# Kernel optimization log

Hardware: AMD Instinct MI355X
Metric: run time of the kernel (lower is better)

The kernel has to match this reference:

```python
import jax, jax.numpy as jnp
import numpy as np


def setup_inputs() -> dict:
    key = jax.random.key(0)
    k1, k2, k3 = jax.random.split(key, 3)
    B, C, H, W = 8, 256, 64, 64
    K = jax.random.normal(k1, (B, C, H, W), dtype=jnp.float32)
    Q = jax.random.normal(k2, (B, C, H, W), dtype=jnp.float32)
    V = jax.random.normal(k3, (B, C, H, W), dtype=jnp.float32)
    return {"K": K, "Q": Q, "V": V}


def reference(K, Q, V):
    # K, Q: [b, dim, h, w]; V: [b, v_dim, h, w]
    b, dim, h, w = K.shape
    v_dim = V.shape[1]
    hw = h * w
    Qf = jnp.transpose(K.reshape(b, dim, hw), (0, 2, 1)) * 0  # placeholder removed below
    Qf = jnp.transpose(Q.reshape(b, dim, hw), (0, 2, 1))  # [b, hw, dim]
    Kf = K.reshape(b, dim, hw)                              # [b, dim, hw]
    Vf = jnp.transpose(V.reshape(b, v_dim, hw), (0, 2, 1))  # [b, hw, v_dim]
    scores = jnp.einsum('bqd,bdk->bqk', Qf, Kf)             # [b, hw_q, hw_k]
    # NOTE: softmax over the QUERY axis (dim=1), matching the torch code
    att = jax.nn.softmax(scores, axis=1)
    out = jnp.einsum('bqk,bkv->bqv', att, Vf)               # [b, hw, v_dim]
    out = out.reshape(b, h, w, v_dim)
    return jnp.transpose(out, (0, 3, 1, 2))                 # [b, v_dim, h, w]
```

## Files before the change

### kernel.cpp

```cpp
#include <hip/hip_runtime.h>

#define HW   4096
#define DIM  256
#define NB   8

typedef short bf16x8 __attribute__((ext_vector_type(8)));
typedef short s16x4  __attribute__((ext_vector_type(4)));
typedef float f32x4  __attribute__((ext_vector_type(4)));
typedef float f32x16 __attribute__((ext_vector_type(16)));
typedef unsigned int u32_g __attribute__((address_space(1)));
typedef unsigned int u32_l __attribute__((address_space(3)));

__device__ __forceinline__ void split_bf16(float x, short& hi, short& lo) {
    unsigned u  = __builtin_bit_cast(unsigned, x);
    unsigned rh = (u + 0x7FFFu + ((u >> 16) & 1u)) >> 16;
    hi = (short)rh;
    float hf  = __builtin_bit_cast(float, rh << 16);
    float rem = x - hf;
    unsigned u2 = __builtin_bit_cast(unsigned, rem);
    unsigned rl = (u2 + 0x7FFFu + ((u2 >> 16) & 1u)) >> 16;
    lo = (short)rl;
}

__device__ __forceinline__ f32x4 mfma16(bf16x8 a, bf16x8 b, f32x4 c) {
    return __builtin_amdgcn_mfma_f32_16x16x32_bf16(a, b, c, 0, 0, 0);
}
__device__ __forceinline__ f32x16 mfma32(bf16x8 a, bf16x8 b, f32x16 c) {
    return __builtin_amdgcn_mfma_f32_32x32x16_bf16(a, b, c, 0, 0, 0);
}

__device__ __forceinline__ void gload16(const void* g, void* l) {
    __builtin_amdgcn_global_load_lds((const u32_g*)g, (u32_l*)l, 16, 0, 0);
}
__device__ __forceinline__ void gload4(const void* g, void* l) {
    __builtin_amdgcn_global_load_lds((const u32_g*)g, (u32_l*)l, 4, 0, 0);
}

extern "C" __global__ void __launch_bounds__(256)
pass0_T(const float* __restrict__ src, short* __restrict__ dsth,
        short* __restrict__ dstl)
{
    __shared__ __attribute__((aligned(16))) short TH[16][264];
    __shared__ __attribute__((aligned(16))) short TL[16][264];
    const int b   = blockIdx.y;
    const int hw0 = blockIdx.x * 16;
    const int t   = threadIdx.x;
    const float* sb = src + (size_t)b * DIM * HW;

    {
        const int rl = t & 15;
        const int dl = t >> 4;
        #pragma unroll
        for (int dp = 0; dp < 16; ++dp) {
            int d = dl + dp * 16;
            float x = sb[(size_t)d * HW + hw0 + rl];
            short h, l; split_bf16(x, h, l);
            TH[rl][d] = h; TL[rl][d] = l;
        }
    }
    __syncthreads();

    const int r   = t >> 4;
    const int c0  = (t & 15) * 2;
    const int swz = r << 4;
    size_t rowbyte = ((size_t)b * HW + hw0 + r) * (size_t)(DIM * 2);
    char* dh = (char*)dsth + rowbyte;
    char* dl = (char*)dstl + rowbyte;
    #pragma unroll
    for (int j = 0; j < 2; ++j) {
        int cb  = (c0 + j) * 16;
        int cbs = cb ^ swz;
        *(f32x4*)(dh + cbs) = *(const f32x4*)((const char*)&TH[r][0] + cb);
        *(f32x4*)(dl + cbs) = *(const f32x4*)((const char*)&TL[r][0] + cb);
    }
}

extern "C" __global__ void __launch_bounds__(256)
pass0_V(const float* __restrict__ V, short* __restrict__ v2)
{
    const int b = blockIdx.y, v = blockIdx.x, t = threadIdx.x;
    const float* sv = V + ((size_t)b * DIM + v) * HW + t * 16;
    #pragma unroll
    for (int s = 0; s < 2; ++s) {
        f32x4 x0 = *(const f32x4*)(sv + s * 8);
        f32x4 x1 = *(const f32x4*)(sv + s * 8 + 4);
        s16x4 h0, l0, h1, l1;
        #pragma unroll
        for (int j = 0; j < 4; ++j) {
            short h, l;
            split_bf16(x0[j], h, l); h0[j] = h; l0[j] = l;
            split_bf16(x1[j], h, l); h1[j] = h; l1[j] = l;
        }
        short* dp = v2 + (((size_t)b * 512 + (size_t)(t * 2 + s)) * DIM + v) * 16;
        *(s16x4*)(dp + 0)  = h0;
        *(s16x4*)(dp + 4)  = h1;
        *(s16x4*)(dp + 8)  = l0;
        *(s16x4*)(dp + 12) = l1;
    }
}

extern "C" __global__ void __launch_bounds__(512, 2)
k9_stats(const short* __restrict__ KTh, const short* __restrict__ KTl,
         const short* __restrict__ QTh, const short* __restrict__ QTl,
         float* __restrict__ m_out, float* __restrict__ il_out)
{
    __shared__ __attribute__((aligned(16))) short QH[2][64][256];
    __shared__ __attribute__((aligned(16))) short QL[2][64][256];
    __shared__ __attribute__((aligned(16))) float MRG[2][128][2];

    const int id   = blockIdx.x;
    const int b    = id & 7;
    const int k0b  = (id >> 3) * 128;
    const int t    = threadIdx.x;
    const int lane = t & 63;
    const int w    = t >> 6;
    const int l32  = lane & 31;
    const int g2   = lane >> 5;
    const int wk   = w >> 1;
    const int wq   = w & 1;

    bf16x8 kh[16], kl[16];
    {
        const int krow = k0b + wk * 32 + l32;
        const char* rh = (const char*)KTh + ((size_t)b * HW + krow) * 512;
        const char* rl = (const char*)KTl + ((size_t)b * HW + krow) * 512;
        const int swz = (l32 & 15) << 4;
        #pragma unroll
        for (int s = 0; s < 16; ++s) {
            int cb = (s * 32 + g2 * 16) ^ swz;
            kh[s] = *(const bf16x8*)(rh + cb);
            kl[s] = *(const bf16x8*)(rl + cb);
        }
    }

    const char* qhbase = (const char*)QTh + (size_t)b * HW * 512;
    const char* qlbase = (const char*)QTl + (size_t)b * HW * 512;
    auto stage = [&](int bi, int q0s) {
        #pragma unroll
        for (int j = 0; j < 4; ++j) {
            int cc = (j << 3) + w;
            int o  = cc * 1024;
            gload16(qhbase + (size_t)q0s * 512 + o + lane * 16,
                    (char*)&QH[bi][0][0] + o);
            gload16(qlbase + (size_t)q0s * 512 + o + lane * 16,
                    (char*)&QL[bi][0][0] + o);
        }
    };

    const int qrow = wq * 32 + l32;
    const int qswz = (l32 & 15) << 4;

    float mr[16], lr[16];
    #pragma unroll
    for (int r = 0; r < 16; ++r) { mr[r] = -3.0e38f; lr[r] = 0.0f; }

    stage(0, 0);
    __syncthreads();

    for (int it = 0; it < 64; ++it) {
        const int cur = it & 1;
        if (it + 1 < 64) stage(cur ^ 1, (it + 1) * 64);

        const char* bhr = (const char*)&QH[cur][qrow][0];
        const char* blr = (const char*)&QL[cur][qrow][0];
        f32x16 cS;
        #pragma unroll
        for (int e = 0; e < 16; ++e) cS[e] = 0.0f;

        __builtin_amdgcn_s_setprio(1);
        #pragma unroll
        for (int s = 0; s < 16; ++s) {
            int cb = (s * 32 + g2 * 16) ^ qswz;
            bf16x8 bh = *(const bf16x8*)(bhr + cb);
            bf16x8 bl = *(const bf16x8*)(blr + cb);
            cS = mfma32(kh[s], bh, cS);
            cS = mfma32(kh[s], bl, cS);
            cS = mfma32(kl[s], bh, cS);
        }
        __builtin_amdgcn_s_setprio(0);

        #pragma unroll
        for (int r = 0; r < 16; ++r) {
            float sv = cS[r];
            float nm = fmaxf(mr[r], sv);
            lr[r] = lr[r] * __expf(mr[r] - nm) + __expf(sv - nm);
            mr[r] = nm;
        }
        __syncthreads();
    }

    #pragma unroll
    for (int r = 0; r < 16; ++r) {
        float m = mr[r], l = lr[r];
        #pragma unroll
        for (int off = 1; off < 32; off <<= 1) {
            float m2 = __shfl_xor(m, off);
            float l2 = __shfl_xor(l, off);
            float nm = fmaxf(m, m2);
            l = l * __expf(m - nm) + l2 * __expf(m2 - nm);
            m = nm;
        }
        mr[r] = m; lr[r] = l;
    }
    if (l32 == 0) {
        #pragma unroll
        for (int r = 0; r < 16; ++r) {
            int klo = wk * 32 + 4 * g2 + (r & 3) + 8 * (r >> 2);
            MRG[wq][klo][0] = mr[r];
            MRG[wq][klo][1] = lr[r];
        }
    }
    __syncthreads();
    if (t < 128) {
        float m0 = MRG[0][t][0], l0 = MRG[0][t][1];
        float m1 = MRG[1][t][0], l1 = MRG[1][t][1];
        float nm = fmaxf(m0, m1);
        float l  = l0 * __expf(m0 - nm) + l1 * __expf(m1 - nm);
        m_out[b * HW + k0b + t]  = nm;
        il_out[b * HW + k0b + t] = 1.0f / l;
    }
}

extern "C" __global__ void __launch_bounds__(512, 2)
k9_out(const short* __restrict__ KTh, const short* __restrict__ KTl,
       const short* __restrict__ QTh, const short* __restrict__ QTl,
       const short* __restrict__ V2,
       const float* __restrict__ m_in, const float* __restrict__ il_in,
       float* __restrict__ out)
{
    __shared__ __attribute__((aligned(16))) short KH[2][64][256];
    __shared__ __attribute__((aligned(16))) short KL[64][256];
    __shared__ __attribute__((aligned(16))) short PH[128][68];
    __shared__ __attribute__((aligned(16))) short PL[128][68];
    __shared__ __attribute__((aligned(16))) float MI[2][128];

    const int id   = blockIdx.x;
    const int b    = id & 7;
    const int q0   = (id >> 3) * 128;
    const int t    = threadIdx.x;
    const int lane = t & 63;
    const int w    = t >> 6;
    const int l32  = lane & 31;
    const int g2   = lane >> 5;
    const int a    = w & 1;
    const int c    = w >> 1;
    const int wv   = w >> 1;
    const int wq2  = w & 1;

    bf16x8 qh[16], ql[16];
    {
        const int qrow = q0 + c * 32 + l32;
        const char* rh = (const char*)QTh + ((size_t)b * HW + qrow) * 512;
        const char* rl = (const char*)QTl + ((size_t)b * HW + qrow) * 512;
        const int swz = (l32 & 15) << 4;
        #pragma unroll
        for (int s = 0; s < 16; ++s) {
            int cb = (s * 32 + g2 * 16) ^ swz;
            qh[s] = *(const bf16x8*)(rh + cb);
            ql[s] = *(const bf16x8*)(rl + cb);
        }
    }

    const char* khbase = (const char*)KTh + (size_t)b * HW * 512;
    const char* klbase = (const char*)KTl + (size_t)b * HW * 512;
    auto stageKH = [&](int bi, int k0s) {
        #pragma unroll
        for (int j = 0; j < 4; ++j) {
            int cc = (j << 3) + w;
            int o  = cc * 1024;
            gload16(khbase + (size_t)k0s * 512 + o + lane * 16,
                    (char*)&KH[bi][0][0] + o);
        }
    };
    auto stageKL = [&](int k0s) {
        #pragma unroll
        for (int j = 0; j < 4; ++j) {
            int cc = (j << 3) + w;
            int o  = cc * 1024;
            gload16(klbase + (size_t)k0s * 512 + o + lane * 16,
                    (char*)&KL[0][0] + o);
        }
    };
    const float* mB  = m_in  + b * HW;
    const float* ilB = il_in + b * HW;
    auto stageMI = [&](int bi, int k0s) {
        if (w == 0) {
            gload4(mB  + k0s + lane, (char*)&MI[bi][0]);
            gload4(ilB + k0s + lane, (char*)&MI[bi][64]);
        }
    };

    f32x16 acc[2][2];
    #pragma unroll
    for (int i = 0; i < 2; ++i)
        #pragma unroll
        for (int j = 0; j < 2; ++j)
            #pragma unroll
            for (int e = 0; e < 16; ++e) acc[i][j][e] = 0.0f;

    stageKH(0, 0);
    stageKL(0);
    stageMI(0, 0);
    __syncthreads();

    const int arow = a * 32 + l32;
    const int aswz = (l32 & 15) << 4;
    const int prow = c * 32 + l32;

    for (int it = 0; it < 64; ++it) {
        const int cur = it & 1;
        const int k0  = it * 64;

        if (it + 1 < 64) {
            stageKH(cur ^ 1, k0 + 64);
            stageMI(cur ^ 1, k0 + 64);
        }
        bf16x8 v0h[2], v0l[2];
        {
            const int seg = it * 8 + g2;
            #pragma unroll
            for (int mt = 0; mt < 2; ++mt) {
                int v = wv * 64 + mt * 32 + l32;
                const short* vp = V2 + (((size_t)b * 512 + seg) * DIM + v) * 16;
                v0h[mt] = *(const bf16x8*)(vp);
                v0l[mt] = *(const bf16x8*)(vp + 8);
            }
        }

        const char* ahr = (const char*)&KH[cur][arow][0];
        const char* alr = (const char*)&KL[arow][0];
        f32x16 cS;
        #pragma unroll
        for (int e = 0; e < 16; ++e) cS[e] = 0.0f;

        __builtin_amdgcn_s_setprio(1);
        #pragma unroll
        for (int s = 0; s < 16; ++s) {
            int cb = (s * 32 + g2 * 16) ^ aswz;
            bf16x8 ah = *(const bf16x8*)(ahr + cb);
            bf16x8 al = *(const bf16x8*)(alr + cb);
            cS = mfma32(ah, qh[s], cS);
            cS = mfma32(ah, ql[s], cS);
            cS = mfma32(al, qh[s], cS);
        }
        __builtin_amdgcn_s_setprio(0);

        __syncthreads();

        if (it + 1 < 64) stageKL(k0 + 64);

        #pragma unroll
        for (int run = 0; run < 4; ++run) {
            int idx = a * 32 + 4 * g2 + 8 * run;
            f32x4 m4 = *(const f32x4*)&MI[cur][idx];
            f32x4 i4 = *(const f32x4*)&MI[cur][64 + idx];
            s16x4 ph, pl;
            #pragma unroll
            for (int e = 0; e < 4; ++e) {
                int r = run * 4 + e;
                float p = __expf(cS[r] - m4[e]) * i4[e];
                short h, l; split_bf16(p, h, l);
                ph[e] = h; pl[e] = l;
            }
            *(s16x4*)&PH[prow][idx] = ph;
            *(s16x4*)&PL[prow][idx] = pl;
        }

        __syncthreads();

        __builtin_amdgcn_s_setprio(1);
        #pragma unroll
        for (int kc = 0; kc < 4; ++kc) {
            bf16x8 pbh[2], pbl[2];
            #pragma unroll
            for (int qt = 0; qt < 2; ++qt) {
                int pr = wq2 * 64 + qt * 32 + l32;
                const short* p0 = &PH[pr][kc * 16 + g2 * 8];
                const short* p1 = &PL[pr][kc * 16 + g2 * 8];
                s16x4 a0 = *(const s16x4*)(p0);
                s16x4 a1 = *(const s16x4*)(p0 + 4);
                s16x4 b0 = *(const s16x4*)(p1);
                s16x4 b1 = *(const s16x4*)(p1 + 4);
                pbh[qt] = __builtin_shufflevector(a0, a1, 0, 1, 2, 3, 4, 5, 6, 7);
                pbl[qt] = __builtin_shufflevector(b0, b1, 0, 1, 2, 3, 4, 5, 6, 7);
            }
            const int seg = it * 8 + kc * 2 + g2;
            #pragma unroll
            for (int mt = 0; mt < 2; ++mt) {
                bf16x8 vh, vl;
                if (kc == 0) {
                    vh = v0h[mt]; vl = v0l[mt];
                } else {
                    int v = wv * 64 + mt * 32 + l32;
                    const short* vp = V2 + (((size_t)b * 512 + seg) * DIM + v) * 16;
                    vh = *(const bf16x8*)(vp);
                    vl = *(const bf16x8*)(vp + 8);
                }
                #pragma unroll
                for (int qt = 0; qt < 2; ++qt) {
                    acc[mt][qt] = mfma32(vh, pbh[qt], acc[mt][qt]);
                    acc[mt][qt] = mfma32(vh, pbl[qt], acc[mt][qt]);
                    acc[mt][qt] = mfma32(vl, pbh[qt], acc[mt][qt]);
                }
            }
        }
        __builtin_amdgcn_s_setprio(0);
    }

    float* __restrict__ ob = out + (size_t)b * DIM * HW;
    #pragma unroll
    for (int mt = 0; mt < 2; ++mt)
        #pragma unroll
        for (int qt = 0; qt < 2; ++qt)
            #pragma unroll
            for (int r = 0; r < 16; ++r) {
                int v = wv * 64 + mt * 32 + (r & 3) + 8 * (r >> 2) + 4 * g2;
                int q = q0 + wq2 * 64 + qt * 32 + l32;
                ob[(size_t)v * HW + q] = acc[mt][qt][r];
            }
}

extern "C" __global__ void __launch_bounds__(256, 1)
k_stats(const float* __restrict__ K, const float* __restrict__ Q,
        float* __restrict__ m_out, float* __restrict__ il_out)
{
    __shared__ __attribute__((aligned(16))) short KtH[64][264];
    __shared__ __attribute__((aligned(16))) short KtL[64][264];
    __shared__ __attribute__((aligned(16))) short QtH[32][264];
    __shared__ __attribute__((aligned(16))) short QtL[32][264];

    const int b = blockIdx.y, k0 = blockIdx.x * 64, t = threadIdx.x;
    const int lane = t & 63, w = t >> 6, g = lane >> 4, lq = lane & 15;
    const float* Kb = K + (size_t)b * DIM * HW;
    const float* Qb = Q + (size_t)b * DIM * HW;

    {
        const int kk = t & 63, d0 = t >> 6;
        #pragma unroll 4
        for (int pass = 0; pass < 64; ++pass) {
            int d = d0 + pass * 4;
            float x = Kb[(size_t)d * HW + k0 + kk];
            short h, l; split_bf16(x, h, l);
            KtH[kk][d] = h; KtL[kk][d] = l;
        }
    }
    float mr[4], lr[4];
    #pragma unroll
    for (int r = 0; r < 4; ++r) { mr[r] = -3.0e38f; lr[r] = 0.0f; }

    for (int q0 = 0; q0 < HW; q0 += 32) {
        __syncthreads();
        {
            const int qq = t & 31, d0 = t >> 5;
            #pragma unroll 4
            for (int pass = 0; pass < 32; ++pass) {
                int d = d0 + pass * 8;
                float x = Qb[(size_t)d * HW + q0 + qq];
                short h, l; split_bf16(x, h, l);
                QtH[qq][d] = h; QtL[qq][d] = l;
            }
        }
        __syncthreads();
        #pragma unroll
        for (int qt = 0; qt < 2; ++qt) {
            f32x4 acc = {0.f, 0.f, 0.f, 0.f};
            #pragma unroll
            for (int ds = 0; ds < 8; ++ds) {
                const int dof = ds * 32 + g * 8;
                bf16x8 ah = *(const bf16x8*)&KtH[w * 16 + lq][dof];
                bf16x8 al = *(const bf16x8*)&KtL[w * 16 + lq][dof];
                bf16x8 bh = *(const bf16x8*)&QtH[qt * 16 + lq][dof];
                bf16x8 bl = *(const bf16x8*)&QtL[qt * 16 + lq][dof];
                acc = mfma16(ah, bh, acc);
                acc = mfma16(ah, bl, acc);
                acc = mfma16(al, bh, acc);
            }
            #pragma unroll
            for (int r = 0; r < 4; ++r) {
                float s = acc[r];
                if (s > mr[r]) { lr[r] = lr[r] * __expf(mr[r] - s) + 1.0f; mr[r] = s; }
                else lr[r] += __expf(s - mr[r]);
            }
        }
    }
    #pragma unroll
    for (int r = 0; r < 4; ++r) {
        float m = mr[r], l = lr[r];
        #pragma unroll
        for (int off = 1; off < 16; off <<= 1) {
            float m2 = __shfl_xor(m, off), l2 = __shfl_xor(l, off);
            float mn = fmaxf(m, m2);
            l = l * __expf(m - mn) + l2 * __expf(m2 - mn);
            m = mn;
        }
        if (lq == 0) {
            int kg = k0 + w * 16 + g * 4 + r;
            m_out[b * HW + kg] = m;
            il_out[b * HW + kg] = 1.0f / l;
        }
    }
}

extern "C" __global__ void __launch_bounds__(256, 1)
k_attn_out(const float* __restrict__ K, const float* __restrict__ Q,
           const float* __restrict__ V,
           const float* __restrict__ m_in, const float* __restrict__ il_in,
           float* __restrict__ out)
{
    __shared__ __attribute__((aligned(16))) short QtH[64][264];
    __shared__ __attribute__((aligned(16))) short QtL[64][264];
    __shared__ __attribute__((aligned(16))) short KtH[32][264];
    __shared__ __attribute__((aligned(16))) short KtL[32][264];
    __shared__ __attribute__((aligned(16))) short PtH[64][40];
    __shared__ __attribute__((aligned(16))) short PtL[64][40];

    const int b = blockIdx.y, q0 = blockIdx.x * 64, t = threadIdx.x;
    const int lane = t & 63, w = t >> 6, g = lane >> 4, lq = lane & 15;
    const int g2 = lane >> 5, l32 = lane & 31;
    const float* Kb = K + (size_t)b * DIM * HW;
    const float* Qb = Q + (size_t)b * DIM * HW;
    const float* Vb = V + (size_t)b * DIM * HW;
    const float* mB = m_in + b * HW;
    const float* ilB = il_in + b * HW;

    {
        const int qq = t & 63, d0 = t >> 6;
        #pragma unroll 4
        for (int pass = 0; pass < 64; ++pass) {
            int d = d0 + pass * 4;
            float x = Qb[(size_t)d * HW + q0 + qq];
            short h, l; split_bf16(x, h, l);
            QtH[qq][d] = h; QtL[qq][d] = l;
        }
    }
    f32x16 acc[2][2];
    #pragma unroll
    for (int i = 0; i < 2; ++i)
        #pragma unroll
        for (int j = 0; j < 2; ++j)
            #pragma unroll
            for (int e = 0; e < 16; ++e) acc[i][j][e] = 0.0f;

    for (int k0 = 0; k0 < HW; k0 += 32) {
        __syncthreads();
        {
            const int kk = t & 31, d0 = t >> 5;
            #pragma unroll 4
            for (int pass = 0; pass < 32; ++pass) {
                int d = d0 + pass * 8;
                float x = Kb[(size_t)d * HW + k0 + kk];
                short h, l; split_bf16(x, h, l);
                KtH[kk][d] = h; KtL[kk][d] = l;
            }
        }
        __syncthreads();
        f32x4 sacc[2];
        #pragma unroll
        for (int kt = 0; kt < 2; ++kt) { f32x4 z = {0.f,0.f,0.f,0.f}; sacc[kt] = z; }
        #pragma unroll
        for (int ds = 0; ds < 8; ++ds) {
            const int dof = ds * 32 + g * 8;
            bf16x8 bh = *(const bf16x8*)&QtH[w * 16 + lq][dof];
            bf16x8 bl = *(const bf16x8*)&QtL[w * 16 + lq][dof];
            #pragma unroll
            for (int kt = 0; kt < 2; ++kt) {
                bf16x8 ah = *(const bf16x8*)&KtH[kt * 16 + lq][dof];
                bf16x8 al = *(const bf16x8*)&KtL[kt * 16 + lq][dof];
                sacc[kt] = mfma16(ah, bh, sacc[kt]);
                sacc[kt] = mfma16(ah, bl, sacc[kt]);
                sacc[kt] = mfma16(al, bh, sacc[kt]);
            }
        }
        {
            const int qc = w * 16 + lq;
            #pragma unroll
            for (int kt = 0; kt < 2; ++kt) {
                s16x4 ph, pl;
                #pragma unroll
                for (int r = 0; r < 4; ++r) {
                    int kg = k0 + kt * 16 + g * 4 + r;
                    float p = __expf(sacc[kt][r] - mB[kg]) * ilB[kg];
                    short h, l; split_bf16(p, h, l);
                    ph[r] = h; pl[r] = l;
                }
                *(s16x4*)&PtH[qc][kt * 16 + g * 4] = ph;
                *(s16x4*)&PtL[qc][kt * 16 + g * 4] = pl;
            }
        }
        __syncthreads();
        #pragma unroll
        for (int kc = 0; kc < 2; ++kc) {
            bf16x8 pbh[2], pbl[2];
            #pragma unroll
            for (int qt = 0; qt < 2; ++qt) {
                pbh[qt] = *(const bf16x8*)&PtH[qt * 32 + l32][kc * 16 + g2 * 8];
                pbl[qt] = *(const bf16x8*)&PtL[qt * 32 + l32][kc * 16 + g2 * 8];
            }
            #pragma unroll
            for (int mt = 0; mt < 2; ++mt) {
                const int v = w * 64 + mt * 32 + l32;
                const float* vp = Vb + (size_t)v * HW + k0 + kc * 16 + g2 * 8;
                f32x4 x0 = *(const f32x4*)vp;
                f32x4 x1 = *(const f32x4*)(vp + 4);
                bf16x8 ah, al;
                #pragma unroll
                for (int j = 0; j < 4; ++j) {
                    short h, l;
                    split_bf16(x0[j], h, l); ah[j] = h;     al[j] = l;
                    split_bf16(x1[j], h, l); ah[4 + j] = h; al[4 + j] = l;
                }
                #pragma unroll
                for (int qt = 0; qt < 2; ++qt) {
                    acc[mt][qt] = mfma32(ah, pbh[qt], acc[mt][qt]);
                    acc[mt][qt] = mfma32(ah, pbl[qt], acc[mt][qt]);
                    acc[mt][qt] = mfma32(al, pbh[qt], acc[mt][qt]);
                }
            }
        }
    }
    float* ob = out + (size_t)b * DIM * HW;
    #pragma unroll
    for (int mt = 0; mt < 2; ++mt)
        #pragma unroll
        for (int qt = 0; qt < 2; ++qt)
            #pragma unroll
            for (int r = 0; r < 16; ++r) {
                int v = w * 64 + mt * 32 + (r & 3) + 8 * (r >> 2) + 4 * g2;
                int q = q0 + qt * 32 + l32;
                ob[(size_t)v * HW + q] = acc[mt][qt][r];
            }
}

extern "C" void kernel_launch(void* const* d_in, const int* in_sizes, int n_in,
                              void* d_out, int out_size, void* d_ws, size_t ws_size,
                              hipStream_t stream)
{
    (void)in_sizes; (void)n_in; (void)out_size;
    const float* K = (const float*)d_in[0];
    const float* Q = (const float*)d_in[1];
    const float* V = (const float*)d_in[2];

    char* wsb = (char*)d_ws;
    float* m_ws  = (float*)wsb;
    float* il_ws = m_ws + (size_t)NB * HW;

    const size_t planeElems = (size_t)NB * HW * DIM;
    const size_t statsBytes = 262144;
    const size_t need = statsBytes + planeElems * 2 * 4
                                   + planeElems * 2 * 2 ;

    dim3 blk(256);
    if (ws_size >= need) {
        short* KTh = (short*)(wsb + statsBytes);
        short* KTl = KTh + planeElems;
        short* QTh = KTl + planeElems;
        short* QTl = QTh + planeElems;
        short* V2  = QTl + planeElems;

        dim3 gT(HW / 16, NB);
        pass0_T<<<gT, blk, 0, stream>>>(K, KTh, KTl);
        pass0_T<<<gT, blk, 0, stream>>>(Q, QTh, QTl);
        dim3 gV(DIM, NB);
        pass0_V<<<gV, blk, 0, stream>>>(V, V2);

        dim3 blk5(512);
        k9_stats<<<dim3(256), blk5, 0, stream>>>(KTh, KTl, QTh, QTl, m_ws, il_ws);
        k9_out<<<dim3(256), blk5, 0, stream>>>(KTh, KTl, QTh, QTl, V2,
                                               m_ws, il_ws, (float*)d_out);
    } else {
        dim3 gM(64, NB);
        k_stats<<<gM, blk, 0, stream>>>(K, Q, m_ws, il_ws);
        k_attn_out<<<gM, blk, 0, stream>>>(K, Q, V, m_ws, il_ws, (float*)d_out);
    }
}
```

Before: 703.6 us.

## Warp-specialize output kernel into QK producer and PV consumer waves

The output kernel is split so four waves compute QK scores and softmax probabilities while the other four load K tiles and run the PV matmul for the previous tile, overlapping the two stages across iterations. The per-block query tile is halved to 64 and the grid doubled to 512 blocks. KL becomes double-buffered and staging moves entirely to the consumer waves. This aims to hide the latency between the score and PV phases, but halves the per-wave matmul parallelism and grows the LDS footprint, which may reduce occupancy.

```diff
diff --git a/kernel.cpp b/kernel.cpp
--- a/kernel.cpp
+++ b/kernel.cpp
@@ -222,33 +222,34 @@
 }
 
 extern "C" __global__ void __launch_bounds__(512, 2)
-k9_out(const short* __restrict__ KTh, const short* __restrict__ KTl,
-       const short* __restrict__ QTh, const short* __restrict__ QTl,
-       const short* __restrict__ V2,
-       const float* __restrict__ m_in, const float* __restrict__ il_in,
-       float* __restrict__ out)
+k10_out(const short* __restrict__ KTh, const short* __restrict__ KTl,
+        const short* __restrict__ QTh, const short* __restrict__ QTl,
+        const short* __restrict__ V2,
+        const float* __restrict__ m_in, const float* __restrict__ il_in,
+        float* __restrict__ out)
 {
     __shared__ __attribute__((aligned(16))) short KH[2][64][256];
-    __shared__ __attribute__((aligned(16))) short KL[64][256];
-    __shared__ __attribute__((aligned(16))) short PH[128][68];
-    __shared__ __attribute__((aligned(16))) short PL[128][68];
+    __shared__ __attribute__((aligned(16))) short KL[2][64][256];
+    __shared__ __attribute__((aligned(16))) short PH[64][68];
+    __shared__ __attribute__((aligned(16))) short PL[64][68];
     __shared__ __attribute__((aligned(16))) float MI[2][128];
 
     const int id   = blockIdx.x;
     const int b    = id & 7;
-    const int q0   = (id >> 3) * 128;
+    const int q0   = (id >> 3) * 64;
     const int t    = threadIdx.x;
     const int lane = t & 63;
     const int w    = t >> 6;
     const int l32  = lane & 31;
     const int g2   = lane >> 5;
+    const bool producer = (w < 4);
     const int a    = w & 1;
     const int c    = w >> 1;
-    const int wv   = w >> 1;
-    const int wq2  = w & 1;
+    const int cw   = w - 4;
+    const int wv   = cw;
 
     bf16x8 qh[16], ql[16];
-    {
+    if (producer) {
         const int qrow = q0 + c * 32 + l32;
         const char* rh = (const char*)QTh + ((size_t)b * HW + qrow) * 512;
         const char* rl = (const char*)QTl + ((size_t)b * HW + qrow) * 512;
@@ -263,28 +264,22 @@
 
     const char* khbase = (const char*)KTh + (size_t)b * HW * 512;
     const char* klbase = (const char*)KTl + (size_t)b * HW * 512;
-    auto stageKH = [&](int bi, int k0s) {
-        #pragma unroll
-        for (int j = 0; j < 4; ++j) {
-            int cc = (j << 3) + w;
+    const float* mB   = m_in  + b * HW;
+    const float* ilB  = il_in + b * HW;
+
+    auto stageK = [&](int bi, int k0s) {
+        #pragma unroll
+        for (int j = 0; j < 8; ++j) {
+            int cc = (j << 2) + cw;
             int o  = cc * 1024;
             gload16(khbase + (size_t)k0s * 512 + o + lane * 16,
                     (char*)&KH[bi][0][0] + o);
+            gload16(klbase + (size_t)k0s * 512 + o + lane * 16,
+                    (char*)&KL[bi][0][0] + o);
         }
     };
-    auto stageKL = [&](int k0s) {
-        #pragma unroll
-        for (int j = 0; j < 4; ++j) {
-            int cc = (j << 3) + w;
-            int o  = cc * 1024;
-            gload16(klbase + (size_t)k0s * 512 + o + lane * 16,
-                    (char*)&KL[0][0] + o);
-        }
-    };
-    const float* mB  = m_in  + b * HW;
-    const float* ilB = il_in + b * HW;
     auto stageMI = [&](int bi, int k0s) {
-        if (w == 0) {
+        if (w == 4) {
             gload4(mB  + k0s + lane, (char*)&MI[bi][0]);
             gload4(ilB + k0s + lane, (char*)&MI[bi][64]);
         }
@@ -298,126 +293,151 @@
             #pragma unroll
             for (int e = 0; e < 16; ++e) acc[i][j][e] = 0.0f;
 
-    stageKH(0, 0);
-    stageKL(0);
-    stageMI(0, 0);
+    if (!producer) {
+        stageK(0, 0);
+        stageMI(0, 0);
+    }
     __syncthreads();
 
     const int arow = a * 32 + l32;
     const int aswz = (l32 & 15) << 4;
     const int prow = c * 32 + l32;
 
+    s16x4 phr[4], plr[4];
+    bf16x8 pbh[4][2], pbl[4][2];
+
+    auto pvStep = [&](int pit, int kc, const bf16x8* bh2, const bf16x8* bl2) {
+        const int seg = pit * 8 + kc * 2 + g2;
+        #pragma unroll
+        for (int mt = 0; mt < 2; ++mt) {
+            int v = wv * 64 + mt * 32 + l32;
+            const short* vp = V2 + (((size_t)b * 512 + seg) * DIM + v) * 16;
+            bf16x8 vh = *(const bf16x8*)(vp);
+            bf16x8 vl = *(const bf16x8*)(vp + 8);
+            #pragma unroll
+            for (int qt = 0; qt < 2; ++qt) {
+                acc[mt][qt] = mfma32(vh, bh2[qt], acc[mt][qt]);
+                acc[mt][qt] = mfma32(vh, bl2[qt], acc[mt][qt]);
+                acc[mt][qt] = mfma32(vl, bh2[qt], acc[mt][qt]);
+            }
+        }
+    };
+
     for (int it = 0; it < 64; ++it) {
         const int cur = it & 1;
-        const int k0  = it * 64;
-
-        if (it + 1 < 64) {
-            stageKH(cur ^ 1, k0 + 64);
-            stageMI(cur ^ 1, k0 + 64);
-        }
-        bf16x8 v0h[2], v0l[2];
-        {
-            const int seg = it * 8 + g2;
-            #pragma unroll
-            for (int mt = 0; mt < 2; ++mt) {
-                int v = wv * 64 + mt * 32 + l32;
-                const short* vp = V2 + (((size_t)b * 512 + seg) * DIM + v) * 16;
-                v0h[mt] = *(const bf16x8*)(vp);
-                v0l[mt] = *(const bf16x8*)(vp + 8);
-            }
-        }
-
-        const char* ahr = (const char*)&KH[cur][arow][0];
-        const char* alr = (const char*)&KL[arow][0];
-        f32x16 cS;
-        #pragma unroll
-        for (int e = 0; e < 16; ++e) cS[e] = 0.0f;
-
-        __builtin_amdgcn_s_setprio(1);
-        #pragma unroll
-        for (int s = 0; s < 16; ++s) {
-            int cb = (s * 32 + g2 * 16) ^ aswz;
-            bf16x8 ah = *(const bf16x8*)(ahr + cb);
-            bf16x8 al = *(const bf16x8*)(alr + cb);
-            cS = mfma32(ah, qh[s], cS);
-            cS = mfma32(ah, ql[s], cS);
-            cS = mfma32(al, qh[s], cS);
-        }
-        __builtin_amdgcn_s_setprio(0);
-
-        __syncthreads();
-
-        if (it + 1 < 64) stageKL(k0 + 64);
-
-        #pragma unroll
-        for (int run = 0; run < 4; ++run) {
-            int idx = a * 32 + 4 * g2 + 8 * run;
-            f32x4 m4 = *(const f32x4*)&MI[cur][idx];
-            f32x4 i4 = *(const f32x4*)&MI[cur][64 + idx];
-            s16x4 ph, pl;
-            #pragma unroll
-            for (int e = 0; e < 4; ++e) {
-                int r = run * 4 + e;
-                float p = __expf(cS[r] - m4[e]) * i4[e];
-                short h, l; split_bf16(p, h, l);
-                ph[e] = h; pl[e] = l;
-            }
-            *(s16x4*)&PH[prow][idx] = ph;
-            *(s16x4*)&PL[prow][idx] = pl;
-        }
-
-        __syncthreads();
-
-        __builtin_amdgcn_s_setprio(1);
-        #pragma unroll
-        for (int kc = 0; kc < 4; ++kc) {
-            bf16x8 pbh[2], pbl[2];
+
+        if (!producer) {
+            if (it + 1 < 64) {
+                stageK(cur ^ 1, (it + 1) * 64);
+                stageMI(cur ^ 1, (it + 1) * 64);
+            }
+            if (it > 0) {
+                #pragma unroll
+                for (int kc = 0; kc < 4; ++kc)
+                    #pragma unroll
+                    for (int qt = 0; qt < 2; ++qt) {
+                        int pr = qt * 32 + l32;
+                        const short* p0 = &PH[pr][kc * 16 + g2 * 8];
+                        const short* p1 = &PL[pr][kc * 16 + g2 * 8];
+                        s16x4 a0 = *(const s16x4*)(p0);
+                        s16x4 a1 = *(const s16x4*)(p0 + 4);
+                        s16x4 b0 = *(const s16x4*)(p1);
+                        s16x4 b1 = *(const s16x4*)(p1 + 4);
+                        pbh[kc][qt] = __builtin_shufflevector(a0, a1, 0,1,2,3,4,5,6,7);
+                        pbl[kc][qt] = __builtin_shufflevector(b0, b1, 0,1,2,3,4,5,6,7);
+                    }
+                __builtin_amdgcn_s_setprio(1);
+                pvStep(it - 1, 0, pbh[0], pbl[0]);
+                pvStep(it - 1, 1, pbh[1], pbl[1]);
+                __builtin_amdgcn_s_setprio(0);
+            }
+        } else {
+            const char* ahr = (const char*)&KH[cur][arow][0];
+            const char* alr = (const char*)&KL[cur][arow][0];
+            f32x16 cS;
+            #pragma unroll
+            for (int e = 0; e < 16; ++e) cS[e] = 0.0f;
+
+            __builtin_amdgcn_s_setprio(1);
+            #pragma unroll
+            for (int s = 0; s < 16; ++s) {
+                int cb = (s * 32 + g2 * 16) ^ aswz;
+                bf16x8 ah = *(const bf16x8*)(ahr + cb);
+                bf16x8 al = *(const bf16x8*)(alr + cb);
+                cS = mfma32(ah, qh[s], cS);
+                cS = mfma32(ah, ql[s], cS);
+                cS = mfma32(al, qh[s], cS);
+            }
+            __builtin_amdgcn_s_setprio(0);
+
+            #pragma unroll
+            for (int run = 0; run < 4; ++run) {
+                int idx = a * 32 + 4 * g2 + 8 * run;
+                f32x4 m4 = *(const f32x4*)&MI[cur][idx];
+                f32x4 i4 = *(const f32x4*)&MI[cur][64 + idx];
+                s16x4 ph, pl;
+                #pragma unroll
+                for (int e = 0; e < 4; ++e) {
+                    int r = run * 4 + e;
+                    float p = __expf(cS[r] - m4[e]) * i4[e];
+                    short h, l; split_bf16(p, h, l);
+                    ph[e] = h; pl[e] = l;
+                }
+                phr[run] = ph; plr[run] = pl;
+            }
+        }
+
+        __syncthreads();
+
+        if (!producer) {
+            if (it > 0) {
+                __builtin_amdgcn_s_setprio(1);
+                pvStep(it - 1, 2, pbh[2], pbl[2]);
+                pvStep(it - 1, 3, pbh[3], pbl[3]);
+                __builtin_amdgcn_s_setprio(0);
+            }
+        } else {
+            #pragma unroll
+            for (int run = 0; run < 4; ++run) {
+                int idx = a * 32 + 4 * g2 + 8 * run;
+                *(s16x4*)&PH[prow][idx] = phr[run];
+                *(s16x4*)&PL[prow][idx] = plr[run];
+            }
+        }
+
+        __syncthreads();
+    }
+
+    if (!producer) {
+        #pragma unroll
+        for (int kc = 0; kc < 4; ++kc)
             #pragma unroll
             for (int qt = 0; qt < 2; ++qt) {
-                int pr = wq2 * 64 + qt * 32 + l32;
+                int pr = qt * 32 + l32;
                 const short* p0 = &PH[pr][kc * 16 + g2 * 8];
                 const short* p1 = &PL[pr][kc * 16 + g2 * 8];
                 s16x4 a0 = *(const s16x4*)(p0);
                 s16x4 a1 = *(const s16x4*)(p0 + 4);
                 s16x4 b0 = *(const s16x4*)(p1);
                 s16x4 b1 = *(const s16x4*)(p1 + 4);
-                pbh[qt] = __builtin_shufflevector(a0, a1, 0, 1, 2, 3, 4, 5, 6, 7);
-                pbl[qt] = __builtin_shufflevector(b0, b1, 0, 1, 2, 3, 4, 5, 6, 7);
-            }
-            const int seg = it * 8 + kc * 2 + g2;
-            #pragma unroll
-            for (int mt = 0; mt < 2; ++mt) {
-                bf16x8 vh, vl;
-                if (kc == 0) {
-                    vh = v0h[mt]; vl = v0l[mt];
-                } else {
-                    int v = wv * 64 + mt * 32 + l32;
-                    const short* vp = V2 + (((size_t)b * 512 + seg) * DIM + v) * 16;
-                    vh = *(const bf16x8*)(vp);
-                    vl = *(const bf16x8*)(vp + 8);
+                pbh[kc][qt] = __builtin_shufflevector(a0, a1, 0,1,2,3,4,5,6,7);
+                pbl[kc][qt] = __builtin_shufflevector(b0, b1, 0,1,2,3,4,5,6,7);
+            }
+        #pragma unroll
+        for (int kc = 0; kc < 4; ++kc) pvStep(63, kc, pbh[kc], pbl[kc]);
+
+        float* __restrict__ ob = out + (size_t)b * DIM * HW;
+        #pragma unroll
+        for (int mt = 0; mt < 2; ++mt)
+            #pragma unroll
+            for (int qt = 0; qt < 2; ++qt)
+                #pragma unroll
+                for (int r = 0; r < 16; ++r) {
+                    int v = wv * 64 + mt * 32 + (r & 3) + 8 * (r >> 2) + 4 * g2;
+                    int q = q0 + qt * 32 + l32;
+                    ob[(size_t)v * HW + q] = acc[mt][qt][r];
                 }
-                #pragma unroll
-                for (int qt = 0; qt < 2; ++qt) {
-                    acc[mt][qt] = mfma32(vh, pbh[qt], acc[mt][qt]);
-                    acc[mt][qt] = mfma32(vh, pbl[qt], acc[mt][qt]);
-                    acc[mt][qt] = mfma32(vl, pbh[qt], acc[mt][qt]);
-                }
-            }
-        }
-        __builtin_amdgcn_s_setprio(0);
-    }
-
-    float* __restrict__ ob = out + (size_t)b * DIM * HW;
-    #pragma unroll
-    for (int mt = 0; mt < 2; ++mt)
-        #pragma unroll
-        for (int qt = 0; qt < 2; ++qt)
-            #pragma unroll
-            for (int r = 0; r < 16; ++r) {
-                int v = wv * 64 + mt * 32 + (r & 3) + 8 * (r >> 2) + 4 * g2;
-                int q = q0 + wq2 * 64 + qt * 32 + l32;
-                ob[(size_t)v * HW + q] = acc[mt][qt][r];
-            }
+    }
 }
 
 extern "C" __global__ void __launch_bounds__(256, 1)
@@ -665,8 +685,8 @@
 
         dim3 blk5(512);
         k9_stats<<<dim3(256), blk5, 0, stream>>>(KTh, KTl, QTh, QTl, m_ws, il_ws);
-        k9_out<<<dim3(256), blk5, 0, stream>>>(KTh, KTl, QTh, QTl, V2,
-                                               m_ws, il_ws, (float*)d_out);
+        k10_out<<<dim3(512), blk5, 0, stream>>>(KTh, KTl, QTh, QTl, V2,
+                                                m_ws, il_ws, (float*)d_out);
     } else {
         dim3 gM(64, NB);
         k_stats<<<gM, blk, 0, stream>>>(K, Q, m_ws, il_ws);
```

New measurement: 1.266 ms. 80.0% more time.

## Restructure output kernel to 32-key tiles with 16x16 MFMA score computation

Applied to the files above, without the earlier changes.

The output kernel now processes 32 keys per iteration instead of 64. It computes scores with 16x16 MFMAs, so each wave holds only 8 Q fragments per plane instead of 16. The K low plane is now double-buffered together with the high plane, which removes the separate mid-iteration KL staging. This cuts register pressure and simplifies the pipeline. In exchange it doubles the iteration count, and with it the barrier count and MI/P staging overhead per key.

```diff
diff --git a/kernel.cpp b/kernel.cpp
--- a/kernel.cpp
+++ b/kernel.cpp
@@ -222,14 +222,14 @@
 }
 
 extern "C" __global__ void __launch_bounds__(512, 2)
-k9_out(const short* __restrict__ KTh, const short* __restrict__ KTl,
-       const short* __restrict__ QTh, const short* __restrict__ QTl,
-       const short* __restrict__ V2,
-       const float* __restrict__ m_in, const float* __restrict__ il_in,
-       float* __restrict__ out)
+k11_out(const short* __restrict__ KTh, const short* __restrict__ KTl,
+        const short* __restrict__ QTh, const short* __restrict__ QTl,
+        const short* __restrict__ V2,
+        const float* __restrict__ m_in, const float* __restrict__ il_in,
+        float* __restrict__ out)
 {
-    __shared__ __attribute__((aligned(16))) short KH[2][64][256];
-    __shared__ __attribute__((aligned(16))) short KL[64][256];
+    __shared__ __attribute__((aligned(16))) short KH[2][32][256];
+    __shared__ __attribute__((aligned(16))) short KL[2][32][256];
     __shared__ __attribute__((aligned(16))) short PH[128][68];
     __shared__ __attribute__((aligned(16))) short PL[128][68];
     __shared__ __attribute__((aligned(16))) float MI[2][128];
@@ -240,45 +240,38 @@
     const int t    = threadIdx.x;
     const int lane = t & 63;
     const int w    = t >> 6;
+    const int lq   = lane & 15;
+    const int g    = lane >> 4;
     const int l32  = lane & 31;
     const int g2   = lane >> 5;
-    const int a    = w & 1;
-    const int c    = w >> 1;
     const int wv   = w >> 1;
     const int wq2  = w & 1;
 
-    bf16x8 qh[16], ql[16];
+    bf16x8 qh[8], ql[8];
     {
-        const int qrow = q0 + c * 32 + l32;
+        const int qrow = q0 + w * 16 + lq;
         const char* rh = (const char*)QTh + ((size_t)b * HW + qrow) * 512;
         const char* rl = (const char*)QTl + ((size_t)b * HW + qrow) * 512;
-        const int swz = (l32 & 15) << 4;
-        #pragma unroll
-        for (int s = 0; s < 16; ++s) {
-            int cb = (s * 32 + g2 * 16) ^ swz;
-            qh[s] = *(const bf16x8*)(rh + cb);
-            ql[s] = *(const bf16x8*)(rl + cb);
+        const int swz = lq << 4;
+        #pragma unroll
+        for (int ds = 0; ds < 8; ++ds) {
+            int cb = (64 * ds + 16 * g) ^ swz;
+            qh[ds] = *(const bf16x8*)(rh + cb);
+            ql[ds] = *(const bf16x8*)(rl + cb);
         }
     }
 
     const char* khbase = (const char*)KTh + (size_t)b * HW * 512;
     const char* klbase = (const char*)KTl + (size_t)b * HW * 512;
-    auto stageKH = [&](int bi, int k0s) {
-        #pragma unroll
-        for (int j = 0; j < 4; ++j) {
+    auto stageK = [&](int bi, int k0s) {
+        #pragma unroll
+        for (int j = 0; j < 2; ++j) {
             int cc = (j << 3) + w;
             int o  = cc * 1024;
             gload16(khbase + (size_t)k0s * 512 + o + lane * 16,
                     (char*)&KH[bi][0][0] + o);
-        }
-    };
-    auto stageKL = [&](int k0s) {
-        #pragma unroll
-        for (int j = 0; j < 4; ++j) {
-            int cc = (j << 3) + w;
-            int o  = cc * 1024;
             gload16(klbase + (size_t)k0s * 512 + o + lane * 16,
-                    (char*)&KL[0][0] + o);
+                    (char*)&KL[bi][0][0] + o);
         }
     };
     const float* mB  = m_in  + b * HW;
@@ -298,26 +291,24 @@
             #pragma unroll
             for (int e = 0; e < 16; ++e) acc[i][j][e] = 0.0f;
 
-    stageKH(0, 0);
-    stageKL(0);
+    stageK(0, 0);
     stageMI(0, 0);
     __syncthreads();
 
-    const int arow = a * 32 + l32;
-    const int aswz = (l32 & 15) << 4;
-    const int prow = c * 32 + l32;
-
-    for (int it = 0; it < 64; ++it) {
+    const int swzk = lq << 4;
+    const int prow = w * 16 + lq;
+
+    for (int it = 0; it < 128; ++it) {
         const int cur = it & 1;
-        const int k0  = it * 64;
-
-        if (it + 1 < 64) {
-            stageKH(cur ^ 1, k0 + 64);
-            stageMI(cur ^ 1, k0 + 64);
+        const int k0  = it * 32;
+
+        if (it + 1 < 128) {
+            stageK(cur ^ 1, k0 + 32);
+            stageMI(cur ^ 1, k0 + 32);
         }
         bf16x8 v0h[2], v0l[2];
         {
-            const int seg = it * 8 + g2;
+            const int seg = it * 4 + g2;
             #pragma unroll
             for (int mt = 0; mt < 2; ++mt) {
                 int v = wv * 64 + mt * 32 + l32;
@@ -327,40 +318,50 @@
             }
         }
 
-        const char* ahr = (const char*)&KH[cur][arow][0];
-        const char* alr = (const char*)&KL[arow][0];
-        f32x16 cS;
-        #pragma unroll
-        for (int e = 0; e < 16; ++e) cS[e] = 0.0f;
+        const char* ahr0 = (const char*)&KH[cur][lq][0];
+        const char* ahr1 = (const char*)&KH[cur][16 + lq][0];
+        const char* alr0 = (const char*)&KL[cur][lq][0];
+        const char* alr1 = (const char*)&KL[cur][16 + lq][0];
+        f32x4 sacc[2];
+        #pragma unroll
+        for (int kt = 0; kt < 2; ++kt) { f32x4 z = {0.f,0.f,0.f,0.f}; sacc[kt] = z; }
 
         __builtin_amdgcn_s_setprio(1);
         #pragma unroll
-        for (int s = 0; s < 16; ++s) {
-            int cb = (s * 32 + g2 * 16) ^ aswz;
-            bf16x8 ah = *(const bf16x8*)(ahr + cb);
-            bf16x8 al = *(const bf16x8*)(alr + cb);
-            cS = mfma32(ah, qh[s], cS);
-            cS = mfma32(ah, ql[s], cS);
-            cS = mfma32(al, qh[s], cS);
+        for (int ds = 0; ds < 8; ++ds) {
+            int cb = (64 * ds + 16 * g) ^ swzk;
+            bf16x8 bh = qh[ds];
+            bf16x8 bl = ql[ds];
+            {
+                bf16x8 ah = *(const bf16x8*)(ahr0 + cb);
+                bf16x8 al = *(const bf16x8*)(alr0 + cb);
+                sacc[0] = mfma16(ah, bh, sacc[0]);
+                sacc[0] = mfma16(ah, bl, sacc[0]);
+                sacc[0] = mfma16(al, bh, sacc[0]);
+            }
+            {
+                bf16x8 ah = *(const bf16x8*)(ahr1 + cb);
+                bf16x8 al = *(const bf16x8*)(alr1 + cb);
+                sacc[1] = mfma16(ah, bh, sacc[1]);
+                sacc[1] = mfma16(ah, bl, sacc[1]);
+                sacc[1] = mfma16(al, bh, sacc[1]);
+            }
         }
         __builtin_amdgcn_s_setprio(0);
 
         __syncthreads();
 
-        if (it + 1 < 64) stageKL(k0 + 64);
-
-        #pragma unroll
-        for (int run = 0; run < 4; ++run) {
-            int idx = a * 32 + 4 * g2 + 8 * run;
+        #pragma unroll
+        for (int kt = 0; kt < 2; ++kt) {
+            int idx = kt * 16 + g * 4;
             f32x4 m4 = *(const f32x4*)&MI[cur][idx];
             f32x4 i4 = *(const f32x4*)&MI[cur][64 + idx];
             s16x4 ph, pl;
             #pragma unroll
-            for (int e = 0; e < 4; ++e) {
-                int r = run * 4 + e;
-                float p = __expf(cS[r] - m4[e]) * i4[e];
+            for (int r = 0; r < 4; ++r) {
+                float p = __expf(sacc[kt][r] - m4[r]) * i4[r];
                 short h, l; split_bf16(p, h, l);
-                ph[e] = h; pl[e] = l;
+                ph[r] = h; pl[r] = l;
             }
             *(s16x4*)&PH[prow][idx] = ph;
             *(s16x4*)&PL[prow][idx] = pl;
@@ -370,7 +371,7 @@
 
         __builtin_amdgcn_s_setprio(1);
         #pragma unroll
-        for (int kc = 0; kc < 4; ++kc) {
+        for (int kc = 0; kc < 2; ++kc) {
             bf16x8 pbh[2], pbl[2];
             #pragma unroll
             for (int qt = 0; qt < 2; ++qt) {
@@ -384,7 +385,7 @@
                 pbh[qt] = __builtin_shufflevector(a0, a1, 0, 1, 2, 3, 4, 5, 6, 7);
                 pbl[qt] = __builtin_shufflevector(b0, b1, 0, 1, 2, 3, 4, 5, 6, 7);
             }
-            const int seg = it * 8 + kc * 2 + g2;
+            const int seg = it * 4 + kc * 2 + g2;
             #pragma unroll
             for (int mt = 0; mt < 2; ++mt) {
                 bf16x8 vh, vl;
@@ -665,8 +666,8 @@
 
         dim3 blk5(512);
         k9_stats<<<dim3(256), blk5, 0, stream>>>(KTh, KTl, QTh, QTl, m_ws, il_ws);
-        k9_out<<<dim3(256), blk5, 0, stream>>>(KTh, KTl, QTh, QTl, V2,
-                                               m_ws, il_ws, (float*)d_out);
+        k11_out<<<dim3(256), blk5, 0, stream>>>(KTh, KTl, QTh, QTl, V2,
+                                                m_ws, il_ws, (float*)d_out);
     } else {
         dim3 gM(64, NB);
         k_stats<<<gM, blk, 0, stream>>>(K, Q, m_ws, il_ws);
```

Result: faster. 651.1 us (-7.5%).
